# Kernel tuning notes

Measured on AMD Instinct MI355X. Metric: run time of the kernel, lower is better.

The kernel has to match this reference:

```python
import jax, jax.numpy as jnp
import numpy as np

T = 4096      # sentence length
V = 50257     # vocab size
E = 1024      # embedding dim
H = 512       # hidden per direction (hidden_dim // 2)
NT = 32       # tagset size


def setup_inputs() -> dict:
    key = jax.random.key(0)
    ks = jax.random.split(key, 12)
    s = 0.02
    return {
        "sentence": jax.random.randint(ks[0], (T,), 0, V, dtype=jnp.int32),
        "emb": jax.random.normal(ks[1], (V, E), jnp.float32) * s,
        "W_ih_f": jax.random.normal(ks[2], (3 * H, E), jnp.float32) * s,
        "W_hh_f": jax.random.normal(ks[3], (3 * H, H), jnp.float32) * s,
        "b_ih_f": jax.random.normal(ks[4], (3 * H,), jnp.float32) * s,
        "b_hh_f": jax.random.normal(ks[5], (3 * H,), jnp.float32) * s,
        "W_ih_b": jax.random.normal(ks[6], (3 * H, E), jnp.float32) * s,
        "W_hh_b": jax.random.normal(ks[7], (3 * H, H), jnp.float32) * s,
        "b_ih_b": jax.random.normal(ks[8], (3 * H,), jnp.float32) * s,
        "b_hh_b": jax.random.normal(ks[9], (3 * H,), jnp.float32) * s,
        "W_out": jax.random.normal(ks[10], (NT, E), jnp.float32) * s,
    }


def _gru_dir(x, W_ih, W_hh, b_ih, b_hh):
    """Run a single-direction GRU over x [T, E] -> hidden states [T, H].
    PyTorch GRU gate math: r,z,n order; h' = (1-z)*n + z*h; h0 = 0."""
    gi = x @ W_ih.T + b_ih  # [T, 3H] input projections, one big GEMM

    def step(h, gi_t):
        gh = h @ W_hh.T + b_hh            # [3H]
        ir, iz, inn = jnp.split(gi_t, 3)
        hr, hz, hn = jnp.split(gh, 3)
        r = jax.nn.sigmoid(ir + hr)
        z = jax.nn.sigmoid(iz + hz)
        n = jnp.tanh(inn + r * hn)
        h_new = (1.0 - z) * n + z * h
        return h_new, h_new

    h0 = jnp.zeros((W_hh.shape[1],), x.dtype)
    _, hs = jax.lax.scan(step, h0, gi)
    return hs  # [T, H]


def reference(sentence, emb, W_ih_f, W_hh_f, b_ih_f, b_hh_f,
              W_ih_b, W_hh_b, b_ih_b, b_hh_b, W_out):
    x = emb[sentence]  # [T, E] embedding lookup
    h_fwd = _gru_dir(x, W_ih_f, W_hh_f, b_ih_f, b_hh_f)            # [T, H]
    h_bwd = _gru_dir(x[::-1], W_ih_b, W_hh_b, b_ih_b, b_hh_b)[::-1]  # [T, H]
    h = jnp.concatenate([h_fwd, h_bwd], axis=-1)  # [T, 2H]
    return h @ W_out.T  # [T, NT] tag scores (no bias)
```

## Files before the change

### kernel.cpp

```cpp
#include <hip/hip_runtime.h>

#define T_LEN 4096
#define E_DIM 1024
#define H_DIM 512
#define NT_DIM 32
#define NG 3072
#define G_DIR 64

typedef __attribute__((ext_vector_type(8))) short bf16x8;
typedef __attribute__((ext_vector_type(4))) float f32x4;
typedef unsigned long long ull;

__device__ inline unsigned short f2bf(float f) {
    unsigned int u = __float_as_uint(f);
    unsigned int r = (u + 0x7fffu + ((u >> 16) & 1u)) >> 16;
    return (unsigned short)r;
}
__device__ inline float bf2f(unsigned short u) {
    return __uint_as_float(((unsigned int)u) << 16);
}
__device__ inline ull packhs(float v, unsigned tag) {
    return (ull)__float_as_uint(v) | ((ull)tag << 32);
}

__global__ void embed_cast(const int* __restrict__ sent, const float* __restrict__ emb,
                           unsigned short* __restrict__ xb) {
    int t = blockIdx.x;
    int row = sent[t];
    const float4* src = (const float4*)(emb + (size_t)row * E_DIM);
    ushort4* dst = (ushort4*)(xb + (size_t)t * E_DIM);
    float4 v = src[threadIdx.x];
    ushort4 o;
    o.x = f2bf(v.x); o.y = f2bf(v.y); o.z = f2bf(v.z); o.w = f2bf(v.w);
    dst[threadIdx.x] = o;
}

__global__ void wcast(const float* __restrict__ wf, const float* __restrict__ wb_,
                      unsigned short* __restrict__ w) {
    int r = blockIdx.x;
    const float* src = (r < 1536) ? (wf + (size_t)r * E_DIM) : (wb_ + (size_t)(r - 1536) * E_DIM);
    const float4* s4 = (const float4*)src;
    ushort4* dst = (ushort4*)(w + (size_t)r * E_DIM);
    float4 v = s4[threadIdx.x];
    ushort4 o;
    o.x = f2bf(v.x); o.y = f2bf(v.y); o.z = f2bf(v.z); o.w = f2bf(v.w);
    dst[threadIdx.x] = o;
}

#define LDST 40
__global__ __launch_bounds__(256) void gi_gemm(const unsigned short* __restrict__ xb,
                                               const unsigned short* __restrict__ wb,
                                               const float* __restrict__ bihf,
                                               const float* __restrict__ bihb,
                                               unsigned short* __restrict__ gi) {
    __shared__ __align__(16) unsigned short As[64 * LDST];
    __shared__ __align__(16) unsigned short Bs[64 * LDST];
    int tile_m = (blockIdx.x % 64) * 64;
    int tile_n = (blockIdx.x / 64) * 64;
    int tid = threadIdx.x;
    int lane = tid & 63, wv = tid >> 6;
    int quad = lane >> 4, r15 = lane & 15;
    int srow = tid >> 2, sseg = tid & 3;

    f32x4 acc[4] = {};
    for (int kb = 0; kb < E_DIM; kb += 32) {
        uint4 a = *(const uint4*)(xb + (size_t)(tile_m + srow) * E_DIM + kb + sseg * 8);
        uint4 b = *(const uint4*)(wb + (size_t)(tile_n + srow) * E_DIM + kb + sseg * 8);
        *(uint4*)&As[srow * LDST + sseg * 8] = a;
        *(uint4*)&Bs[srow * LDST + sseg * 8] = b;
        __syncthreads();
        bf16x8 af = *(bf16x8*)&As[(wv * 16 + r15) * LDST + quad * 8];
#pragma unroll
        for (int nt = 0; nt < 4; nt++) {
            bf16x8 bf = *(bf16x8*)&Bs[(nt * 16 + r15) * LDST + quad * 8];
            acc[nt] = __builtin_amdgcn_mfma_f32_16x16x32_bf16(af, bf, acc[nt], 0, 0, 0);
        }
        __syncthreads();
    }
#pragma unroll
    for (int nt = 0; nt < 4; nt++) {
        int gn = tile_n + nt * 16 + r15;
        float bias = (gn < 1536) ? bihf[gn] : bihb[gn - 1536];
#pragma unroll
        for (int rg = 0; rg < 4; rg++) {
            int gm = tile_m + wv * 16 + quad * 4 + rg;
            gi[(size_t)gm * NG + gn] = f2bf(acc[nt][rg] + bias);
        }
    }
}

__global__ __launch_bounds__(64, 1) void gru_rec(
    const float* __restrict__ whhf, const float* __restrict__ bhhf,
    const float* __restrict__ whhb, const float* __restrict__ bhhb,
    const unsigned short* __restrict__ gi, ull* __restrict__ hxf, ull* __restrict__ hxb) {
    int wgid = blockIdx.x;
    int dir = wgid >> 6;
    int g = wgid & 63;
    const float* whh = dir ? whhb : whhf;
    const float* bhh = dir ? bhhb : bhhf;
    ull* hx = dir ? hxb : hxf;

    int l = threadIdx.x;
    int p = l & 7;
    int o = l >> 3;
    int c = g * 8 + o;

    float4 wr[16], wz[16], wn[16];
    {
        const float4* r0 = (const float4*)(whh + (size_t)c * H_DIM + p * 64);
        const float4* z0 = (const float4*)(whh + (size_t)(c + 512) * H_DIM + p * 64);
        const float4* n0 = (const float4*)(whh + (size_t)(c + 1024) * H_DIM + p * 64);
#pragma unroll
        for (int j = 0; j < 16; j++) { wr[j] = r0[j]; wz[j] = z0[j]; wn[j] = n0[j]; }
    }
    float bias_r = 0.f, bias_z = 0.f, bias_n = 0.f, h_own = 0.f;
    if (p == 0) { bias_r = bhh[c]; bias_z = bhh[c + 512]; bias_n = bhh[c + 1024]; }

    __shared__ float hsh[8 * 68];
#pragma unroll
    for (int i = 0; i < 8; i++) hsh[i * 68 + l] = 0.f;
    __syncthreads();

    float gir = 0.f, giz = 0.f, gin = 0.f;

    for (int s = 0; s < T_LEN; s++) {
        int row = dir ? (T_LEN - 1 - s) : s;
        if (p == 0) {
            const unsigned short* gp = gi + (size_t)row * NG + dir * 1536 + c;
            gir = bf2f(gp[0]); giz = bf2f(gp[512]); gin = bf2f(gp[1024]);
        }
        if (s > 0) {
            int prow = dir ? (T_LEN - s) : (s - 1);
            const ull* rowp = hx + (size_t)prow * H_DIM;
            ull v[8];
            bool ok;
            do {
#pragma unroll
                for (int i = 0; i < 8; i++)
                    v[i] = __hip_atomic_load(rowp + l + 64 * i,
                                             __ATOMIC_RELAXED, __HIP_MEMORY_SCOPE_AGENT);
                ok = true;
#pragma unroll
                for (int i = 0; i < 8; i++)
                    ok = ok && ((unsigned)(v[i] >> 32) == (unsigned)s);
            } while (!ok);
            __syncthreads();
#pragma unroll
            for (int i = 0; i < 8; i++)
                hsh[i * 68 + l] = __uint_as_float((unsigned)v[i]);
        }
        __syncthreads();

        float pr = 0.f, pz = 0.f, pn = 0.f;
        const float* hb = &hsh[p * 68];
#pragma unroll
        for (int j = 0; j < 16; j++) {
            float4 h4 = *(const float4*)(hb + j * 4);
            pr += wr[j].x * h4.x + wr[j].y * h4.y + wr[j].z * h4.z + wr[j].w * h4.w;
            pz += wz[j].x * h4.x + wz[j].y * h4.y + wz[j].z * h4.z + wz[j].w * h4.w;
            pn += wn[j].x * h4.x + wn[j].y * h4.y + wn[j].z * h4.z + wn[j].w * h4.w;
        }
        pr += __shfl_xor(pr, 1);  pz += __shfl_xor(pz, 1);  pn += __shfl_xor(pn, 1);
        pr += __shfl_xor(pr, 2);  pz += __shfl_xor(pz, 2);  pn += __shfl_xor(pn, 2);
        pr += __shfl_xor(pr, 4);  pz += __shfl_xor(pz, 4);  pn += __shfl_xor(pn, 4);

        if (p == 0) {
            float rr = 1.f / (1.f + __expf(-(gir + pr + bias_r)));
            float zz = 1.f / (1.f + __expf(-(giz + pz + bias_z)));
            float a = gin + rr * (pn + bias_n);
            a = fminf(20.f, fmaxf(-20.f, a));
            float e = __expf(-2.f * a);
            float nn = (1.f - e) / (1.f + e);
            float hnew = (1.f - zz) * nn + zz * h_own;
            h_own = hnew;
            __hip_atomic_store(hx + (size_t)row * H_DIM + c, packhs(hnew, (unsigned)(s + 1)),
                               __ATOMIC_RELAXED, __HIP_MEMORY_SCOPE_AGENT);
        }
    }
}

__global__ __launch_bounds__(256) void out_gemm(const ull* __restrict__ hxf,
                                                const ull* __restrict__ hxb,
                                                const float* __restrict__ wout,
                                                float* __restrict__ out) {
    __shared__ __align__(16) float ls[8][1028];
    int t0 = blockIdx.x * 8;
    int tid = threadIdx.x;
#pragma unroll
    for (int i = 0; i < 8; i++) {
        int col = tid * 4;
        const ull* src = (col < 512) ? (hxf + (size_t)(t0 + i) * H_DIM + col)
                                     : (hxb + (size_t)(t0 + i) * H_DIM + (col - 512));
        ull s0 = src[0], s1 = src[1], s2 = src[2], s3 = src[3];
        ls[i][col + 0] = __uint_as_float((unsigned)s0);
        ls[i][col + 1] = __uint_as_float((unsigned)s1);
        ls[i][col + 2] = __uint_as_float((unsigned)s2);
        ls[i][col + 3] = __uint_as_float((unsigned)s3);
    }
    __syncthreads();
    int r8 = tid >> 5, gg = tid & 31;
    const float4* wp = (const float4*)(wout + (size_t)gg * 1024);
    float sum = 0.f;
#pragma unroll 8
    for (int j = 0; j < 256; j++) {
        float4 w = wp[j];
        float4 h = *(const float4*)&ls[r8][j * 4];
        sum += w.x * h.x + w.y * h.y + w.z * h.z + w.w * h.w;
    }
    out[(size_t)(t0 + r8) * NT_DIM + gg] = sum;
}

extern "C" void kernel_launch(void* const* d_in, const int* in_sizes, int n_in,
                              void* d_out, int out_size, void* d_ws, size_t ws_size,
                              hipStream_t stream) {
    const int*   sent = (const int*)d_in[0];
    const float* emb  = (const float*)d_in[1];
    const float* wihf = (const float*)d_in[2];
    const float* whhf = (const float*)d_in[3];
    const float* bihf = (const float*)d_in[4];
    const float* bhhf = (const float*)d_in[5];
    const float* wihb = (const float*)d_in[6];
    const float* whhb = (const float*)d_in[7];
    const float* bihb = (const float*)d_in[8];
    const float* bhhb = (const float*)d_in[9];
    const float* wout = (const float*)d_in[10];

    char* ws = (char*)d_ws;
    unsigned short* gi  = (unsigned short*)(ws);
    unsigned short* xb  = (unsigned short*)(ws + 25165824);
    unsigned short* wb  = (unsigned short*)(ws + 33554432);
    ull*            hxf = (ull*)(ws + 39845888);
    ull*            hxb = (ull*)(ws + 56623104);
    float*          out = (float*)d_out;

    embed_cast<<<T_LEN, 256, 0, stream>>>(sent, emb, xb);
    wcast<<<NG, 256, 0, stream>>>(wihf, wihb, wb);
    gi_gemm<<<64 * 48, 256, 0, stream>>>(xb, wb, bihf, bihb, gi);
    gru_rec<<<2 * G_DIR, 64, 0, stream>>>(whhf, bhhf, whhb, bhhb, gi, hxf, hxb);
    out_gemm<<<T_LEN / 8, 256, 0, stream>>>(hxf, hxb, wout, out);
}
```

Measured before the change: 6.759 ms.

## Restructure GRU recurrence to per-wave two-column ownership with barrier-free polling

Each block now has four independent waves, and each wave owns two hidden columns instead of a block owning eight. Each lane holds an 8-element slice of the full K dimension for those columns and reduces across the whole wave with shuffles. The hidden state is read straight from global memory into registers, with two overlapping batches of polling loads in flight, so the shared-memory staging and the __syncthreads barriers are gone. The goal is to spread the serial recurrence over four times as many waves and cut per-step synchronization latency. The cost is more global polling traffic per step and a longer shuffle-reduction chain.

```diff
diff --git a/kernel.cpp b/kernel.cpp
--- a/kernel.cpp
+++ b/kernel.cpp
@@ -5,7 +5,6 @@
 #define H_DIM 512
 #define NT_DIM 32
 #define NG 3072
-#define G_DIR 64
 
 typedef __attribute__((ext_vector_type(8))) short bf16x8;
 typedef __attribute__((ext_vector_type(4))) float f32x4;
@@ -89,82 +88,107 @@
     }
 }
 
-__global__ __launch_bounds__(64, 1) void gru_rec(
+__global__ __launch_bounds__(256, 1) void gru_rec(
     const float* __restrict__ whhf, const float* __restrict__ bhhf,
     const float* __restrict__ whhb, const float* __restrict__ bhhb,
     const unsigned short* __restrict__ gi, ull* __restrict__ hxf, ull* __restrict__ hxb) {
-    int wgid = blockIdx.x;
-    int dir = wgid >> 6;
-    int g = wgid & 63;
+    int dir = blockIdx.x >> 6;
+    int gw  = (blockIdx.x & 63) * 4 + (threadIdx.x >> 6);
+    int l   = threadIdx.x & 63;
+    int c0  = gw * 2;
     const float* whh = dir ? whhb : whhf;
     const float* bhh = dir ? bhhb : bhhf;
     ull* hx = dir ? hxb : hxf;
 
-    int l = threadIdx.x;
-    int p = l & 7;
-    int o = l >> 3;
-    int c = g * 8 + o;
-
-    float4 wr[16], wz[16], wn[16];
-    {
-        const float4* r0 = (const float4*)(whh + (size_t)c * H_DIM + p * 64);
-        const float4* z0 = (const float4*)(whh + (size_t)(c + 512) * H_DIM + p * 64);
-        const float4* n0 = (const float4*)(whh + (size_t)(c + 1024) * H_DIM + p * 64);
-#pragma unroll
-        for (int j = 0; j < 16; j++) { wr[j] = r0[j]; wz[j] = z0[j]; wn[j] = n0[j]; }
+    float4 wA[6], wB[6];
+#pragma unroll
+    for (int g3 = 0; g3 < 3; g3++) {
+        const float4* pa = (const float4*)(whh + (size_t)(c0 + g3 * 512) * H_DIM + 8 * l);
+        const float4* pb = (const float4*)(whh + (size_t)(c0 + 1 + g3 * 512) * H_DIM + 8 * l);
+        wA[g3 * 2] = pa[0]; wA[g3 * 2 + 1] = pa[1];
+        wB[g3 * 2] = pb[0]; wB[g3 * 2 + 1] = pb[1];
     }
     float bias_r = 0.f, bias_z = 0.f, bias_n = 0.f, h_own = 0.f;
-    if (p == 0) { bias_r = bhh[c]; bias_z = bhh[c + 512]; bias_n = bhh[c + 1024]; }
-
-    __shared__ float hsh[8 * 68];
-#pragma unroll
-    for (int i = 0; i < 8; i++) hsh[i * 68 + l] = 0.f;
-    __syncthreads();
-
-    float gir = 0.f, giz = 0.f, gin = 0.f;
+    if (l < 2) {
+        int c = c0 + l;
+        bias_r = bhh[c]; bias_z = bhh[c + 512]; bias_n = bhh[c + 1024];
+    }
+
+    float h[8];
+#pragma unroll
+    for (int i = 0; i < 8; i++) h[i] = 0.f;
 
     for (int s = 0; s < T_LEN; s++) {
         int row = dir ? (T_LEN - 1 - s) : s;
-        if (p == 0) {
-            const unsigned short* gp = gi + (size_t)row * NG + dir * 1536 + c;
+        float gir = 0.f, giz = 0.f, gin = 0.f;
+        if (l < 2) {
+            const unsigned short* gp = gi + (size_t)row * NG + dir * 1536 + (c0 + l);
             gir = bf2f(gp[0]); giz = bf2f(gp[512]); gin = bf2f(gp[1024]);
         }
+
         if (s > 0) {
             int prow = dir ? (T_LEN - s) : (s - 1);
-            const ull* rowp = hx + (size_t)prow * H_DIM;
-            ull v[8];
-            bool ok;
-            do {
+            const ull* pp = hx + (size_t)prow * H_DIM + 8 * l;
+            unsigned et = (unsigned)s;
+            ull va[8], vb[8], gv[8];
+#pragma unroll
+            for (int i = 0; i < 8; i++)
+                va[i] = __hip_atomic_load(pp + i, __ATOMIC_RELAXED, __HIP_MEMORY_SCOPE_AGENT);
+#pragma unroll
+            for (int i = 0; i < 8; i++)
+                vb[i] = __hip_atomic_load(pp + i, __ATOMIC_RELAXED, __HIP_MEMORY_SCOPE_AGENT);
+            for (;;) {
+                bool ok = true;
+#pragma unroll
+                for (int i = 0; i < 8; i++) ok = ok && ((unsigned)(va[i] >> 32) == et);
+                if (ok) {
+#pragma unroll
+                    for (int i = 0; i < 8; i++) gv[i] = va[i];
+                    break;
+                }
 #pragma unroll
                 for (int i = 0; i < 8; i++)
-                    v[i] = __hip_atomic_load(rowp + l + 64 * i,
-                                             __ATOMIC_RELAXED, __HIP_MEMORY_SCOPE_AGENT);
+                    va[i] = __hip_atomic_load(pp + i, __ATOMIC_RELAXED, __HIP_MEMORY_SCOPE_AGENT);
                 ok = true;
 #pragma unroll
+                for (int i = 0; i < 8; i++) ok = ok && ((unsigned)(vb[i] >> 32) == et);
+                if (ok) {
+#pragma unroll
+                    for (int i = 0; i < 8; i++) gv[i] = vb[i];
+                    break;
+                }
+#pragma unroll
                 for (int i = 0; i < 8; i++)
-                    ok = ok && ((unsigned)(v[i] >> 32) == (unsigned)s);
-            } while (!ok);
-            __syncthreads();
-#pragma unroll
-            for (int i = 0; i < 8; i++)
-                hsh[i * 68 + l] = __uint_as_float((unsigned)v[i]);
-        }
-        __syncthreads();
-
-        float pr = 0.f, pz = 0.f, pn = 0.f;
-        const float* hb = &hsh[p * 68];
-#pragma unroll
-        for (int j = 0; j < 16; j++) {
-            float4 h4 = *(const float4*)(hb + j * 4);
-            pr += wr[j].x * h4.x + wr[j].y * h4.y + wr[j].z * h4.z + wr[j].w * h4.w;
-            pz += wz[j].x * h4.x + wz[j].y * h4.y + wz[j].z * h4.z + wz[j].w * h4.w;
-            pn += wn[j].x * h4.x + wn[j].y * h4.y + wn[j].z * h4.z + wn[j].w * h4.w;
-        }
-        pr += __shfl_xor(pr, 1);  pz += __shfl_xor(pz, 1);  pn += __shfl_xor(pn, 1);
-        pr += __shfl_xor(pr, 2);  pz += __shfl_xor(pz, 2);  pn += __shfl_xor(pn, 2);
-        pr += __shfl_xor(pr, 4);  pz += __shfl_xor(pz, 4);  pn += __shfl_xor(pn, 4);
-
-        if (p == 0) {
+                    vb[i] = __hip_atomic_load(pp + i, __ATOMIC_RELAXED, __HIP_MEMORY_SCOPE_AGENT);
+            }
+#pragma unroll
+            for (int i = 0; i < 8; i++) h[i] = __uint_as_float((unsigned)gv[i]);
+        }
+
+        float prA, pzA, pnA, prB, pzB, pnB;
+        prA = wA[0].x * h[0] + wA[0].y * h[1] + wA[0].z * h[2] + wA[0].w * h[3]
+            + wA[1].x * h[4] + wA[1].y * h[5] + wA[1].z * h[6] + wA[1].w * h[7];
+        pzA = wA[2].x * h[0] + wA[2].y * h[1] + wA[2].z * h[2] + wA[2].w * h[3]
+            + wA[3].x * h[4] + wA[3].y * h[5] + wA[3].z * h[6] + wA[3].w * h[7];
+        pnA = wA[4].x * h[0] + wA[4].y * h[1] + wA[4].z * h[2] + wA[4].w * h[3]
+            + wA[5].x * h[4] + wA[5].y * h[5] + wA[5].z * h[6] + wA[5].w * h[7];
+        prB = wB[0].x * h[0] + wB[0].y * h[1] + wB[0].z * h[2] + wB[0].w * h[3]
+            + wB[1].x * h[4] + wB[1].y * h[5] + wB[1].z * h[6] + wB[1].w * h[7];
+        pzB = wB[2].x * h[0] + wB[2].y * h[1] + wB[2].z * h[2] + wB[2].w * h[3]
+            + wB[3].x * h[4] + wB[3].y * h[5] + wB[3].z * h[6] + wB[3].w * h[7];
+        pnB = wB[4].x * h[0] + wB[4].y * h[1] + wB[4].z * h[2] + wB[4].w * h[3]
+            + wB[5].x * h[4] + wB[5].y * h[5] + wB[5].z * h[6] + wB[5].w * h[7];
+
+#pragma unroll
+        for (int m = 1; m < 64; m <<= 1) {
+            prA += __shfl_xor(prA, m); pzA += __shfl_xor(pzA, m); pnA += __shfl_xor(pnA, m);
+            prB += __shfl_xor(prB, m); pzB += __shfl_xor(pzB, m); pnB += __shfl_xor(pnB, m);
+        }
+
+        if (l < 2) {
+            float pr = l ? prB : prA;
+            float pz = l ? pzB : pzA;
+            float pn = l ? pnB : pnA;
             float rr = 1.f / (1.f + __expf(-(gir + pr + bias_r)));
             float zz = 1.f / (1.f + __expf(-(giz + pz + bias_z)));
             float a = gin + rr * (pn + bias_n);
@@ -173,7 +197,7 @@
             float nn = (1.f - e) / (1.f + e);
             float hnew = (1.f - zz) * nn + zz * h_own;
             h_own = hnew;
-            __hip_atomic_store(hx + (size_t)row * H_DIM + c, packhs(hnew, (unsigned)(s + 1)),
+            __hip_atomic_store(hx + (size_t)row * H_DIM + c0 + l, packhs(hnew, (unsigned)(s + 1)),
                                __ATOMIC_RELAXED, __HIP_MEMORY_SCOPE_AGENT);
         }
     }
@@ -236,6 +260,6 @@
     embed_cast<<<T_LEN, 256, 0, stream>>>(sent, emb, xb);
     wcast<<<NG, 256, 0, stream>>>(wihf, wihb, wb);
     gi_gemm<<<64 * 48, 256, 0, stream>>>(xb, wb, bihf, bihb, gi);
-    gru_rec<<<2 * G_DIR, 64, 0, stream>>>(whhf, bhhf, whhb, bhhb, gi, hxf, hxb);
+    gru_rec<<<128, 256, 0, stream>>>(whhf, bhhf, whhb, bhhb, gi, hxf, hxb);
     out_gemm<<<T_LEN / 8, 256, 0, stream>>>(hxf, hxb, wout, out);
 }
```

Measured after the change: 21.21 ms. 3.14x slower.

## Regroup GRU recurrence into 16 workgroups per direction with single-wave polling

Applied to the files above, without the earlier changes.

Reorganizes the persistent GRU recurrence from 64 single-wave workgroups per direction into 16 workgroups of 8 waves, each computing 32 hidden units. Only wave 0 polls the previous step's hidden row, using wide dwordx4 loads with system-coherent cache bits, then stages it into padded LDS for the other waves. This cuts the number of independent pollers on the global spin barrier and the total polling traffic per step. In exchange it adds an extra block-wide barrier per step and a 16-lane shuffle reduction per hidden unit.

```diff
diff --git a/kernel.cpp b/kernel.cpp
--- a/kernel.cpp
+++ b/kernel.cpp
@@ -5,10 +5,10 @@
 #define H_DIM 512
 #define NT_DIM 32
 #define NG 3072
-#define G_DIR 64
 
 typedef __attribute__((ext_vector_type(8))) short bf16x8;
 typedef __attribute__((ext_vector_type(4))) float f32x4;
+typedef __attribute__((ext_vector_type(4))) unsigned int u32x4;
 typedef unsigned long long ull;
 
 __device__ inline unsigned short f2bf(float f) {
@@ -89,82 +89,93 @@
     }
 }
 
-__global__ __launch_bounds__(64, 1) void gru_rec(
+__global__ __launch_bounds__(512, 2) void gru_rec(
     const float* __restrict__ whhf, const float* __restrict__ bhhf,
     const float* __restrict__ whhb, const float* __restrict__ bhhb,
     const unsigned short* __restrict__ gi, ull* __restrict__ hxf, ull* __restrict__ hxb) {
-    int wgid = blockIdx.x;
-    int dir = wgid >> 6;
-    int g = wgid & 63;
+    int dir = blockIdx.x >> 4;
+    int g   = blockIdx.x & 15;
     const float* whh = dir ? whhb : whhf;
     const float* bhh = dir ? bhhb : bhhf;
     ull* hx = dir ? hxb : hxf;
 
-    int l = threadIdx.x;
-    int p = l & 7;
-    int o = l >> 3;
-    int c = g * 8 + o;
-
-    float4 wr[16], wz[16], wn[16];
-    {
-        const float4* r0 = (const float4*)(whh + (size_t)c * H_DIM + p * 64);
-        const float4* z0 = (const float4*)(whh + (size_t)(c + 512) * H_DIM + p * 64);
-        const float4* n0 = (const float4*)(whh + (size_t)(c + 1024) * H_DIM + p * 64);
-#pragma unroll
-        for (int j = 0; j < 16; j++) { wr[j] = r0[j]; wz[j] = z0[j]; wn[j] = n0[j]; }
-    }
+    int tid = threadIdx.x;
+    int w = tid >> 6;
+    int l = tid & 63;
+    int q = l & 15;
+    int o = l >> 4;
+    int c = g * 32 + w * 4 + o;
+
+    float4 wr[8], wz[8], wn[8];
+#pragma unroll
+    for (int j = 0; j < 8; j++) {
+        wr[j] = *(const float4*)(whh + (size_t)c * H_DIM + q * 32 + j * 4);
+        wz[j] = *(const float4*)(whh + (size_t)(c + 512) * H_DIM + q * 32 + j * 4);
+        wn[j] = *(const float4*)(whh + (size_t)(c + 1024) * H_DIM + q * 32 + j * 4);
+    }
+    bool owner = (q == 0);
     float bias_r = 0.f, bias_z = 0.f, bias_n = 0.f, h_own = 0.f;
-    if (p == 0) { bias_r = bhh[c]; bias_z = bhh[c + 512]; bias_n = bhh[c + 1024]; }
-
-    __shared__ float hsh[8 * 68];
-#pragma unroll
-    for (int i = 0; i < 8; i++) hsh[i * 68 + l] = 0.f;
+    if (owner) { bias_r = bhh[c]; bias_z = bhh[c + 512]; bias_n = bhh[c + 1024]; }
+
+    __shared__ float hsh[576];
+    for (int i = tid; i < 576; i += 512) hsh[i] = 0.f;
     __syncthreads();
-
-    float gir = 0.f, giz = 0.f, gin = 0.f;
 
     for (int s = 0; s < T_LEN; s++) {
         int row = dir ? (T_LEN - 1 - s) : s;
-        if (p == 0) {
+        float gir = 0.f, giz = 0.f, gin = 0.f;
+        if (owner) {
             const unsigned short* gp = gi + (size_t)row * NG + dir * 1536 + c;
             gir = bf2f(gp[0]); giz = bf2f(gp[512]); gin = bf2f(gp[1024]);
         }
-        if (s > 0) {
+
+        float hv[8];
+        if (w == 0 && s > 0) {
             int prow = dir ? (T_LEN - s) : (s - 1);
-            const ull* rowp = hx + (size_t)prow * H_DIM;
-            ull v[8];
-            bool ok;
-            do {
-#pragma unroll
-                for (int i = 0; i < 8; i++)
-                    v[i] = __hip_atomic_load(rowp + l + 64 * i,
-                                             __ATOMIC_RELAXED, __HIP_MEMORY_SCOPE_AGENT);
-                ok = true;
-#pragma unroll
-                for (int i = 0; i < 8; i++)
-                    ok = ok && ((unsigned)(v[i] >> 32) == (unsigned)s);
-            } while (!ok);
-            __syncthreads();
-#pragma unroll
-            for (int i = 0; i < 8; i++)
-                hsh[i * 68 + l] = __uint_as_float((unsigned)v[i]);
+            ull addr = (ull)(hx + (size_t)prow * H_DIM + 8 * l);
+            unsigned et = (unsigned)s;
+            u32x4 d0, d1, d2, d3;
+            for (;;) {
+                asm volatile("global_load_dwordx4 %0, %1, off sc0 sc1" : "=v"(d0) : "v"(addr));
+                asm volatile("global_load_dwordx4 %0, %1, off offset:16 sc0 sc1" : "=v"(d1) : "v"(addr));
+                asm volatile("global_load_dwordx4 %0, %1, off offset:32 sc0 sc1" : "=v"(d2) : "v"(addr));
+                asm volatile("global_load_dwordx4 %0, %1, off offset:48 sc0 sc1" : "=v"(d3) : "v"(addr));
+                asm volatile("s_waitcnt vmcnt(0)" ::: "memory");
+                __builtin_amdgcn_sched_barrier(0);
+                bool ok = (d0.y == et) & (d0.w == et) & (d1.y == et) & (d1.w == et)
+                        & (d2.y == et) & (d2.w == et) & (d3.y == et) & (d3.w == et);
+                if (ok) break;
+            }
+            hv[0] = __uint_as_float(d0.x); hv[1] = __uint_as_float(d0.z);
+            hv[2] = __uint_as_float(d1.x); hv[3] = __uint_as_float(d1.z);
+            hv[4] = __uint_as_float(d2.x); hv[5] = __uint_as_float(d2.z);
+            hv[6] = __uint_as_float(d3.x); hv[7] = __uint_as_float(d3.z);
+        }
+        __syncthreads();
+        if (w == 0 && s > 0) {
+            int base = 8 * l + 4 * (l >> 2);
+            float4 va = { hv[0], hv[1], hv[2], hv[3] };
+            float4 vb = { hv[4], hv[5], hv[6], hv[7] };
+            *(float4*)&hsh[base]     = va;
+            *(float4*)&hsh[base + 4] = vb;
         }
         __syncthreads();
 
         float pr = 0.f, pz = 0.f, pn = 0.f;
-        const float* hb = &hsh[p * 68];
-#pragma unroll
-        for (int j = 0; j < 16; j++) {
-            float4 h4 = *(const float4*)(hb + j * 4);
+        const float* hb = &hsh[36 * q];
+#pragma unroll
+        for (int j = 0; j < 8; j++) {
+            float4 h4 = *(const float4*)(hb + 4 * j);
             pr += wr[j].x * h4.x + wr[j].y * h4.y + wr[j].z * h4.z + wr[j].w * h4.w;
             pz += wz[j].x * h4.x + wz[j].y * h4.y + wz[j].z * h4.z + wz[j].w * h4.w;
             pn += wn[j].x * h4.x + wn[j].y * h4.y + wn[j].z * h4.z + wn[j].w * h4.w;
         }
-        pr += __shfl_xor(pr, 1);  pz += __shfl_xor(pz, 1);  pn += __shfl_xor(pn, 1);
-        pr += __shfl_xor(pr, 2);  pz += __shfl_xor(pz, 2);  pn += __shfl_xor(pn, 2);
-        pr += __shfl_xor(pr, 4);  pz += __shfl_xor(pz, 4);  pn += __shfl_xor(pn, 4);
-
-        if (p == 0) {
+        pr += __shfl_xor(pr, 1); pz += __shfl_xor(pz, 1); pn += __shfl_xor(pn, 1);
+        pr += __shfl_xor(pr, 2); pz += __shfl_xor(pz, 2); pn += __shfl_xor(pn, 2);
+        pr += __shfl_xor(pr, 4); pz += __shfl_xor(pz, 4); pn += __shfl_xor(pn, 4);
+        pr += __shfl_xor(pr, 8); pz += __shfl_xor(pz, 8); pn += __shfl_xor(pn, 8);
+
+        if (owner) {
             float rr = 1.f / (1.f + __expf(-(gir + pr + bias_r)));
             float zz = 1.f / (1.f + __expf(-(giz + pz + bias_z)));
             float a = gin + rr * (pn + bias_n);
@@ -236,6 +247,6 @@
     embed_cast<<<T_LEN, 256, 0, stream>>>(sent, emb, xb);
     wcast<<<NG, 256, 0, stream>>>(wihf, wihb, wb);
     gi_gemm<<<64 * 48, 256, 0, stream>>>(xb, wb, bihf, bihb, gi);
-    gru_rec<<<2 * G_DIR, 64, 0, stream>>>(whhf, bhhf, whhb, bhhb, gi, hxf, hxb);
+    gru_rec<<<32, 512, 0, stream>>>(whhf, bhhf, whhb, bhhb, gi, hxf, hxb);
     out_gemm<<<T_LEN / 8, 256, 0, stream>>>(hxf, hxb, wout, out);
 }
```

Result: slower. 7.291 ms (+7.9%).
